# Optimization experiments

Measured on AMD Instinct MI355X. Metric: run time of the kernel, lower is better.

Reference implementation:

```python
import jax, jax.numpy as jnp
import numpy as np

HEADS = 8
DIM_HEAD = 64
SCALE = DIM_HEAD ** -0.5
EPS = 1e-12  # F.normalize default eps


def setup_inputs() -> dict:
    key = jax.random.key(0)
    ks = jax.random.split(key, 4)
    B, C, H, W = 16, 256, 64, 64
    hidden = HEADS * DIM_HEAD  # 512
    x = jax.random.normal(ks[0], (B, C, H, W), dtype=jnp.float32)
    w_qkv = jax.random.normal(ks[1], (3 * hidden, C), dtype=jnp.float32) * (C ** -0.5)
    w_out = jax.random.normal(ks[2], (C, hidden), dtype=jnp.float32) * (hidden ** -0.5)
    b_out = jax.random.normal(ks[3], (C,), dtype=jnp.float32) * 0.01
    g = jnp.ones((1, C, 1, 1), dtype=jnp.float32)
    return {"x": x, "w_qkv": w_qkv, "w_out": w_out, "b_out": b_out, "g": g}


def reference(x, w_qkv, w_out, b_out, g):
    B, C, H, W = x.shape
    N = H * W
    hidden = HEADS * DIM_HEAD
    # 1x1 conv == channel matmul: [B, 3*hidden, N]
    qkv = jnp.einsum('oc,bcn->bon', w_qkv, x.reshape(B, C, N))
    qkv = qkv.reshape(B, 3, HEADS, DIM_HEAD, N)
    q, k, v = qkv[:, 0], qkv[:, 1], qkv[:, 2]  # each [B, h, d, N]
    q = jax.nn.softmax(q, axis=2) * SCALE      # softmax over channel dim d
    k = jax.nn.softmax(k, axis=3)              # softmax over spatial dim n
    context = jnp.einsum('bhdn,bhen->bhde', k, v)   # [B, h, d, e]
    out = jnp.einsum('bhde,bhdn->bhen', context, q) # [B, h, e, N]
    out = out.reshape(B, hidden, N)
    # to_out: 1x1 conv with bias
    y = jnp.einsum('oc,bcn->bon', w_out, out) + b_out[None, :, None]
    y = y.reshape(B, C, H, W)
    # RMSNorm: F.normalize over channel dim, * g * sqrt(W) (x.shape[-1] == width)
    norm = jnp.sqrt(jnp.sum(y * y, axis=1, keepdims=True))
    y = y / jnp.maximum(norm, EPS)
    return y * g * (W ** 0.5)
```

## Files before the change

### kernel.cpp

```cpp
#include <hip/hip_runtime.h>
#include <hip/hip_bf16.h>

#define NPIX 4096
#define CIN  256
#define HID  512
#define QROWS 1536
#define NB   16

typedef unsigned int u32;
typedef unsigned short u16;
typedef float f32x4 __attribute__((ext_vector_type(4)));
typedef short bf16x8 __attribute__((ext_vector_type(8)));

__device__ __forceinline__ float bf2f(u16 u){
  union { u32 i; float f; } v; v.i = ((u32)u) << 16; return v.f;
}
__device__ __forceinline__ u16 f2bf(float f){
  union { float f; u32 u; } v; v.f = f;
  u32 r = v.u + 0x7fffu + ((v.u >> 16) & 1u);
  return (u16)(r >> 16);
}
__device__ __forceinline__ u32 pkbf(float a, float b){
  __hip_bfloat162 h = __float22bfloat162_rn(make_float2(a, b));
  union { __hip_bfloat162 h; u32 u; } cv; cv.h = h; return cv.u;
}
__device__ __forceinline__ void gload16(const u16* g, u16* l){
  __builtin_amdgcn_global_load_lds(
      (const __attribute__((address_space(1))) void*)g,
      (__attribute__((address_space(3))) void*)l, 16, 0, 0);
}

__global__ void k_marker(float* y, int n){
  int i = blockIdx.x * 256 + threadIdx.x;
  if (i < n) y[i] = 1.0e6f;
}

__global__ __launch_bounds__(256) void k_cvt(const float* __restrict__ src,
                                             u16* __restrict__ dst){
  const int i = (blockIdx.x * 256 + threadIdx.x) * 8;
  const float4 a = *(const float4*)(src + i);
  const float4 b = *(const float4*)(src + i + 4);
  *(uint4*)(dst + i) = make_uint4(pkbf(a.x,a.y), pkbf(a.z,a.w),
                                  pkbf(b.x,b.y), pkbf(b.z,b.w));
}

__global__ __launch_bounds__(256) void k_xt(const float* __restrict__ X,
                                            u16* __restrict__ Xt){
  __shared__ float ls[64][67];
  const int n0 = blockIdx.x * 64, c0 = blockIdx.y * 64, b = blockIdx.z;
  const int tid = threadIdx.x;
  const float* Xb = X + (size_t)b * CIN * NPIX;

  {
    const int r = tid >> 2, cq = (tid & 3) * 16;
    #pragma unroll
    for (int j = 0; j < 4; ++j)
      *(float4*)&ls[r][cq + j*4] = *(const float4*)&Xb[(size_t)(c0 + r) * NPIX + n0 + cq + j*4];
  }
  __syncthreads();
  {
    const int nr = tid >> 2, cs = (tid & 3) * 16;
    u32 pk[8];
    #pragma unroll
    for (int j = 0; j < 8; ++j)
      pk[j] = pkbf(ls[cs + 2*j][nr], ls[cs + 2*j + 1][nr]);
    u16* dst = Xt + (size_t)b * NPIX * CIN + (size_t)(n0 + nr) * CIN + c0 + cs;
    *(uint4*)(dst)     = make_uint4(pk[0], pk[1], pk[2], pk[3]);
    *(uint4*)(dst + 8) = make_uint4(pk[4], pk[5], pk[6], pk[7]);
  }
}

__global__ __launch_bounds__(256, 3) void k_qkv(
    const u16* __restrict__ Wq, const u16* __restrict__ Xt, u16* __restrict__ QKV)
{
  __shared__ __align__(16) u16 pool[17408];
  u16* As = pool;
  u16* Bs = pool + 8192;

  const int flat = blockIdx.x;
  const int virt = (flat & 7) * 768 + (flat >> 3);
  const int o0 = (virt % 12) * 128;
  const int n0 = ((virt / 12) & 31) * 128;
  const int b  = virt / 384;

  const int tid = threadIdx.x;
  const int lane = tid & 63;
  const int wv = tid >> 6;
  const int wr = wv >> 1, wc = wv & 1;
  const int g  = lane >> 4;
  const int c  = lane & 15;
  const u16* Xb = Xt + (size_t)b * NPIX * CIN;

  const int grow = lane >> 3;
  const int gch  = (lane & 7) * 8;

  f32x4 acc[4][4];
  #pragma unroll
  for (int i = 0; i < 4; ++i)
    #pragma unroll
    for (int j = 0; j < 4; ++j) acc[i][j] = (f32x4){0.f, 0.f, 0.f, 0.f};

  for (int s = 0; s < 4; ++s) {
    const int k0 = s * 64;
    #pragma unroll
    for (int i = 0; i < 4; ++i) {
      const int j = wv * 4 + i;
      const int row = j * 8 + grow;
      gload16(&Xb[(size_t)(n0 + row) * CIN + k0 + gch], &As[j * 512]);
      gload16(&Wq[(size_t)(o0 + row) * CIN + k0 + gch], &Bs[j * 512]);
    }
    __syncthreads();

    #pragma unroll
    for (int ks = 0; ks < 2; ++ks) {
      bf16x8 af[4], bfr[4];
      #pragma unroll
      for (int mf = 0; mf < 4; ++mf)
        af[mf] = *(const bf16x8*)&As[(wr * 64 + mf * 16 + c) * 64 + ks * 32 + g * 8];
      #pragma unroll
      for (int nf = 0; nf < 4; ++nf)
        bfr[nf] = *(const bf16x8*)&Bs[(wc * 64 + nf * 16 + c) * 64 + ks * 32 + g * 8];
      #pragma unroll
      for (int mf = 0; mf < 4; ++mf)
        #pragma unroll
        for (int nf = 0; nf < 4; ++nf)
          acc[mf][nf] = __builtin_amdgcn_mfma_f32_16x16x32_bf16(
              af[mf], bfr[nf], acc[mf][nf], 0, 0, 0);
    }
    __syncthreads();
  }

  #pragma unroll
  for (int mf = 0; mf < 4; ++mf) {
    const int nrow = wr * 64 + mf * 16 + g * 4;
    #pragma unroll
    for (int nf = 0; nf < 4; ++nf) {
      const int ocol = wc * 64 + nf * 16 + c;
      #pragma unroll
      for (int r = 0; r < 4; ++r)
        pool[ocol * 136 + nrow + r] = f2bf(acc[mf][nf][r]);
    }
  }
  __syncthreads();
  u16* dst = QKV + (size_t)b * QROWS * NPIX;
  #pragma unroll
  for (int i = 0; i < 8; ++i) {
    const int f2 = i * 256 + tid;
    const int orow = f2 >> 4, ch = f2 & 15;
    const uint4 v = *(const uint4*)&pool[orow * 136 + ch * 8];
    *(uint4*)&dst[(size_t)(o0 + orow) * NPIX + n0 + ch * 8] = v;
  }
}

__global__ __launch_bounds__(256) void k_ctx(const u16* __restrict__ QKV,
    float* __restrict__ ctxp, float* __restrict__ Sp)
{
  __shared__ __align__(16) u16 ks[64 * 72];
  __shared__ __align__(16) u16 vs[64 * 72];
  const int split = blockIdx.x, h = blockIdx.y, b = blockIdx.z;
  const int tid = threadIdx.x;
  const int lane = tid & 63, wv = tid >> 6;
  const int g = lane >> 4, c = lane & 15;
  const u16* kb = QKV + ((size_t)b * QROWS + HID     + h * 64) * NPIX;
  const u16* vb = QKV + ((size_t)b * QROWS + 2 * HID + h * 64) * NPIX;

  const int srow = tid >> 2;
  const int sch  = (tid & 3) * 16;

  f32x4 acc[4];
  #pragma unroll
  for (int j = 0; j < 4; ++j) acc[j] = (f32x4){0.f, 0.f, 0.f, 0.f};
  float s_part = 0.f;

  for (int t = 0; t < 16; ++t) {
    const int n0 = split * 1024 + t * 64;
    {
      const uint4 r0 = *(const uint4*)(kb + (size_t)srow * NPIX + n0 + sch);
      const uint4 r1 = *(const uint4*)(kb + (size_t)srow * NPIX + n0 + sch + 8);
      const u32 w[8] = {r0.x, r0.y, r0.z, r0.w, r1.x, r1.y, r1.z, r1.w};
      u32 pk[8];
      #pragma unroll
      for (int j = 0; j < 8; ++j) {
        const float lo = __expf(bf2f((u16)(w[j] & 0xffff)));
        const float hi = __expf(bf2f((u16)(w[j] >> 16)));
        s_part += lo + hi;
        pk[j] = pkbf(lo, hi);
      }
      *(uint4*)&ks[srow * 72 + sch]     = make_uint4(pk[0], pk[1], pk[2], pk[3]);
      *(uint4*)&ks[srow * 72 + sch + 8] = make_uint4(pk[4], pk[5], pk[6], pk[7]);
      const uint4 v0 = *(const uint4*)(vb + (size_t)srow * NPIX + n0 + sch);
      const uint4 v1 = *(const uint4*)(vb + (size_t)srow * NPIX + n0 + sch + 8);
      *(uint4*)&vs[srow * 72 + sch]     = v0;
      *(uint4*)&vs[srow * 72 + sch + 8] = v1;
    }
    __syncthreads();
    #pragma unroll
    for (int ks2 = 0; ks2 < 2; ++ks2) {
      const bf16x8 af = *(const bf16x8*)&ks[(wv * 16 + c) * 72 + ks2 * 32 + g * 8];
      #pragma unroll
      for (int nf = 0; nf < 4; ++nf) {
        const bf16x8 bf = *(const bf16x8*)&vs[(nf * 16 + c) * 72 + ks2 * 32 + g * 8];
        acc[nf] = __builtin_amdgcn_mfma_f32_16x16x32_bf16(af, bf, acc[nf], 0, 0, 0);
      }
    }
    __syncthreads();
  }
  s_part += __shfl_xor(s_part, 1, 64);
  s_part += __shfl_xor(s_part, 2, 64);
  if ((tid & 3) == 0)
    Sp[(size_t)split * 8192 + (b * 8 + h) * 64 + srow] = s_part;

  float* dst = ctxp + (size_t)split * (NB*8*64*64) + ((size_t)(b*8+h)) * 4096;
  #pragma unroll
  for (int nf = 0; nf < 4; ++nf)
    #pragma unroll
    for (int r = 0; r < 4; ++r)
      dst[(wv*16 + g*4 + r) * 64 + nf*16 + c] = acc[nf][r];
}

__global__ __launch_bounds__(256) void k_ctxred(const float* __restrict__ ctxp,
                                                const float* __restrict__ Sp,
                                                float* __restrict__ ctx)
{
  const int SZ = NB*8*64*64;
  const int i = (blockIdx.x * 256 + threadIdx.x) * 4;
  const int bh = i >> 12, d = (i >> 6) & 63;
  const int si = bh * 64 + d;
  const float S = Sp[si] + Sp[8192 + si] + Sp[16384 + si] + Sp[24576 + si];
  const float inv = 1.0f / S;
  float4 a  = *(const float4*)(ctxp + i);
  const float4 c1 = *(const float4*)(ctxp + SZ   + i);
  const float4 c2 = *(const float4*)(ctxp + 2*SZ + i);
  const float4 c3 = *(const float4*)(ctxp + 3*SZ + i);
  a.x = (a.x + c1.x + c2.x + c3.x) * inv;
  a.y = (a.y + c1.y + c2.y + c3.y) * inv;
  a.z = (a.z + c1.z + c2.z + c3.z) * inv;
  a.w = (a.w + c1.w + c2.w + c3.w) * inv;
  *(float4*)(ctx + i) = a;
}

__global__ __launch_bounds__(256) void k_qctx(u16* __restrict__ QKV,
    const float* __restrict__ ctx)
{
  __shared__ __align__(16) u16 As[256 * 72];
  __shared__ __align__(16) u16 Bs[64 * 72];
  const int nt = blockIdx.x, h = blockIdx.y, b = blockIdx.z;
  const int n0 = nt * 256;
  const int tid = threadIdx.x;
  const int lane = tid & 63, wv = tid >> 6;
  const int g = lane >> 4, c = lane & 15;

  const float* cbase = ctx + ((size_t)(b*8+h)) * 4096;
  #pragma unroll
  for (int j = 0; j < 16; ++j) {
    const int idx = tid + j * 256;
    const int d = idx >> 6, e = idx & 63;
    Bs[e * 72 + d] = f2bf(cbase[idx]);
  }

  const u16* qb = QKV + ((size_t)b*QROWS + h*64) * NPIX;
  float vals[64];
  float mx = -3.0e38f;
  #pragma unroll
  for (int d = 0; d < 64; ++d) {
    vals[d] = bf2f(qb[(size_t)d * NPIX + n0 + tid]);
    mx = fmaxf(mx, vals[d]);
  }
  float s = 0.f;
  #pragma unroll
  for (int d = 0; d < 64; ++d) { vals[d] = __expf(vals[d] - mx); s += vals[d]; }
  const float sc = 0.125f / s;
  #pragma unroll
  for (int q = 0; q < 8; ++q) {
    u32 pk[4];
    #pragma unroll
    for (int p = 0; p < 4; ++p)
      pk[p] = pkbf(vals[q*8 + 2*p] * sc, vals[q*8 + 2*p + 1] * sc);
    *(uint4*)&As[tid * 72 + q * 8] = make_uint4(pk[0], pk[1], pk[2], pk[3]);
  }
  __syncthreads();

  f32x4 acc[4][4];
  #pragma unroll
  for (int i = 0; i < 4; ++i)
    #pragma unroll
    for (int j = 0; j < 4; ++j) acc[i][j] = (f32x4){0.f, 0.f, 0.f, 0.f};
  #pragma unroll
  for (int ks = 0; ks < 2; ++ks) {
    bf16x8 af[4], bfr[4];
    #pragma unroll
    for (int mf = 0; mf < 4; ++mf)
      af[mf] = *(const bf16x8*)&As[(wv * 64 + mf * 16 + c) * 72 + ks * 32 + g * 8];
    #pragma unroll
    for (int nf = 0; nf < 4; ++nf)
      bfr[nf] = *(const bf16x8*)&Bs[(nf * 16 + c) * 72 + ks * 32 + g * 8];
    #pragma unroll
    for (int mf = 0; mf < 4; ++mf)
      #pragma unroll
      for (int nf = 0; nf < 4; ++nf)
        acc[mf][nf] = __builtin_amdgcn_mfma_f32_16x16x32_bf16(
            af[mf], bfr[nf], acc[mf][nf], 0, 0, 0);
  }
  __syncthreads();

  u16* pool = As;
  #pragma unroll
  for (int mf = 0; mf < 4; ++mf) {
    const int nrow = wv * 64 + mf * 16 + g * 4;
    #pragma unroll
    for (int nf = 0; nf < 4; ++nf) {
      const int ecol = nf * 16 + c;
      #pragma unroll
      for (int r = 0; r < 4; ++r)
        pool[ecol * 264 + nrow + r] = f2bf(acc[mf][nf][r]);
    }
  }
  __syncthreads();
  u16* ob = QKV + ((size_t)b*QROWS + h*64) * NPIX;
  #pragma unroll
  for (int i = 0; i < 8; ++i) {
    const int f2 = i * 256 + tid;
    const int erow = f2 >> 5, ch = f2 & 31;
    const uint4 v = *(const uint4*)&pool[erow * 264 + ch * 8];
    *(uint4*)&ob[(size_t)erow * NPIX + n0 + ch * 8] = v;
  }
}

__global__ __launch_bounds__(256) void k_proj(const u16* __restrict__ QKV,
    const u16* __restrict__ Wbf, const float* __restrict__ bo,
    const float* __restrict__ gg, float* __restrict__ Y)
{
  __shared__ __align__(16) u16 As[256][72];
  __shared__ __align__(16) u16 Bs[64][72];
  __shared__ float red[4][64];
  __shared__ float sbias[256], sgain[256];
  const int nt = blockIdx.x, b = blockIdx.y;
  const int n0 = nt * 64;
  const int tid = threadIdx.x;
  const int lane = tid & 63, wv = tid >> 6;
  const int g = lane >> 4, c = lane & 15;
  const u16* ob = QKV + (size_t)b * QROWS * NPIX;

  sbias[tid] = bo[tid];
  sgain[tid] = gg[tid];

  f32x4 acc[4][4];
  #pragma unroll
  for (int i = 0; i < 4; ++i)
    #pragma unroll
    for (int j = 0; j < 4; ++j) acc[i][j] = (f32x4){0.f, 0.f, 0.f, 0.f};

  for (int s = 0; s < 8; ++s) {
    const int k0 = s * 64;
    #pragma unroll
    for (int i = 0; i < 8; ++i) {
      const int flat = i * 256 + tid;
      const int row = flat >> 3, kc = flat & 7;
      *(uint4*)&As[row][kc * 8] =
          *(const uint4*)&Wbf[(size_t)row * HID + k0 + kc * 8];
    }
    {
      const int kb0 = wv * 16;
      u16 vals[16];
      #pragma unroll
      for (int kk = 0; kk < 16; ++kk)
        vals[kk] = ob[(size_t)(k0 + kb0 + kk) * NPIX + n0 + lane];
      u32 pk[8];
      #pragma unroll
      for (int j = 0; j < 8; ++j)
        pk[j] = (u32)vals[2*j] | ((u32)vals[2*j+1] << 16);
      *(uint4*)&Bs[lane][kb0]     = make_uint4(pk[0], pk[1], pk[2], pk[3]);
      *(uint4*)&Bs[lane][kb0 + 8] = make_uint4(pk[4], pk[5], pk[6], pk[7]);
    }
    __syncthreads();

    #pragma unroll
    for (int ks = 0; ks < 2; ++ks) {
      bf16x8 af[4], bfr[4];
      #pragma unroll
      for (int mf = 0; mf < 4; ++mf)
        af[mf] = *(const bf16x8*)&As[wv * 64 + mf * 16 + c][ks * 32 + g * 8];
      #pragma unroll
      for (int nf = 0; nf < 4; ++nf)
        bfr[nf] = *(const bf16x8*)&Bs[nf * 16 + c][ks * 32 + g * 8];
      #pragma unroll
      for (int mf = 0; mf < 4; ++mf)
        #pragma unroll
        for (int nf = 0; nf < 4; ++nf)
          acc[mf][nf] = __builtin_amdgcn_mfma_f32_16x16x32_bf16(
              af[mf], bfr[nf], acc[mf][nf], 0, 0, 0);
    }
    __syncthreads();
  }

  #pragma unroll
  for (int mf = 0; mf < 4; ++mf)
    #pragma unroll
    for (int r = 0; r < 4; ++r) {
      const float bb = sbias[wv * 64 + mf * 16 + g * 4 + r];
      #pragma unroll
      for (int nf = 0; nf < 4; ++nf) acc[mf][nf][r] += bb;
    }

  #pragma unroll
  for (int nf = 0; nf < 4; ++nf) {
    float v = 0.f;
    #pragma unroll
    for (int mf = 0; mf < 4; ++mf)
      #pragma unroll
      for (int r = 0; r < 4; ++r)
        v = fmaf(acc[mf][nf][r], acc[mf][nf][r], v);
    v += __shfl_xor(v, 16, 64);
    v += __shfl_xor(v, 32, 64);
    if (g == 0) red[wv][nf * 16 + c] = v;
  }
  __syncthreads();
  float scale[4];
  #pragma unroll
  for (int nf = 0; nf < 4; ++nf) {
    const int col = nf * 16 + c;
    const float tot = red[0][col] + red[1][col] + red[2][col] + red[3][col];
    scale[nf] = 8.0f / fmaxf(sqrtf(tot), 1e-12f);
  }

  float* yb = Y + (size_t)b * CIN * NPIX;
  #pragma unroll
  for (int mf = 0; mf < 4; ++mf)
    #pragma unroll
    for (int r = 0; r < 4; ++r) {
      const int row = wv * 64 + mf * 16 + g * 4 + r;
      const float gr = sgain[row];
      #pragma unroll
      for (int nf = 0; nf < 4; ++nf)
        yb[(size_t)row * NPIX + n0 + nf * 16 + c] = acc[mf][nf][r] * scale[nf] * gr;
    }
}

extern "C" void kernel_launch(void* const* d_in, const int* in_sizes, int n_in,
                              void* d_out, int out_size, void* d_ws, size_t ws_size,
                              hipStream_t stream) {
  const float* x     = (const float*)d_in[0];
  const float* w_qkv = (const float*)d_in[1];
  const float* w_out = (const float*)d_in[2];
  const float* b_out = (const float*)d_in[3];
  const float* g     = (const float*)d_in[4];
  float* y = (float*)d_out;

  char* ws = (char*)d_ws;
  u16*    qkv   = (u16*)(ws);
  u16*    xt    = (u16*)(ws + 201326592);
  float*  ctx   = (float*)(ws + 201392128);
  float*  ctxp  = (float*)(ws + 203489280);
  float*  Sp    = (float*)(ws + 211877888);
  u16*    wbf   = (u16*)(ws + 234881024);
  u16*    wqb   = (u16*)(ws + 235143168);

  if (ws_size < 235929600) {
    k_marker<<<dim3((out_size + 255) / 256), 256, 0, stream>>>(y, out_size);
    return;
  }

  k_cvt   <<<dim3(64),         256, 0, stream>>>(w_out, wbf);
  k_cvt   <<<dim3(192),        256, 0, stream>>>(w_qkv, wqb);
  k_xt    <<<dim3(64, 4, 16),  256, 0, stream>>>(x, xt);
  k_qkv   <<<dim3(6144),       256, 0, stream>>>(wqb, xt, qkv);
  k_ctx   <<<dim3(4, 8, 16),   256, 0, stream>>>(qkv, ctxp, Sp);
  k_ctxred<<<dim3(512),        256, 0, stream>>>(ctxp, Sp, ctx);
  k_qctx  <<<dim3(16, 8, 16),  256, 0, stream>>>(qkv, ctx);
  k_proj  <<<dim3(64, 16),     256, 0, stream>>>(qkv, wbf, b_out, g, y);
}
```

Baseline: 192.8 us.

## Double-buffer LDS tiles in QKV GEMM to overlap global loads with MFMA

The QKV projection kernel now prefetches the next K-slice of X and W into a second LDS buffer while computing on the current one, using explicit vmcnt waits and raw barriers instead of __syncthreads. This is meant to hide global-to-LDS load latency behind MFMA work. LDS use doubles to 64KB per block, so launch bounds drop from 3 to 2 blocks per CU, which reduces occupancy.

Result: slower. 198.9 us (median of 2 runs) (+3.2%).

```diff
diff --git a/kernel.cpp b/kernel.cpp
--- a/kernel.cpp
+++ b/kernel.cpp
@@ -70,12 +70,10 @@
   }
 }
 
-__global__ __launch_bounds__(256, 3) void k_qkv(
+__global__ __launch_bounds__(256, 2) void k_qkv(
     const u16* __restrict__ Wq, const u16* __restrict__ Xt, u16* __restrict__ QKV)
 {
-  __shared__ __align__(16) u16 pool[17408];
-  u16* As = pool;
-  u16* Bs = pool + 8192;
+  __shared__ __align__(16) u16 lds[32768];
 
   const int flat = blockIdx.x;
   const int virt = (flat & 7) * 768 + (flat >> 3);
@@ -100,17 +98,41 @@
     #pragma unroll
     for (int j = 0; j < 4; ++j) acc[i][j] = (f32x4){0.f, 0.f, 0.f, 0.f};
 
-  for (int s = 0; s < 4; ++s) {
-    const int k0 = s * 64;
+  {
+    u16* As = lds;
+    u16* Bs = lds + 8192;
     #pragma unroll
     for (int i = 0; i < 4; ++i) {
       const int j = wv * 4 + i;
       const int row = j * 8 + grow;
-      gload16(&Xb[(size_t)(n0 + row) * CIN + k0 + gch], &As[j * 512]);
-      gload16(&Wq[(size_t)(o0 + row) * CIN + k0 + gch], &Bs[j * 512]);
-    }
-    __syncthreads();
-
+      gload16(&Xb[(size_t)(n0 + row) * CIN + gch], &As[j * 512]);
+      gload16(&Wq[(size_t)(o0 + row) * CIN + gch], &Bs[j * 512]);
+    }
+  }
+
+  #pragma unroll
+  for (int s = 0; s < 4; ++s) {
+    const int cur = s & 1;
+    if (s < 3) {
+      const int k0 = (s + 1) * 64;
+      u16* As = lds + (cur ^ 1) * 16384;
+      u16* Bs = As + 8192;
+      #pragma unroll
+      for (int i = 0; i < 4; ++i) {
+        const int j = wv * 4 + i;
+        const int row = j * 8 + grow;
+        gload16(&Xb[(size_t)(n0 + row) * CIN + k0 + gch], &As[j * 512]);
+        gload16(&Wq[(size_t)(o0 + row) * CIN + k0 + gch], &Bs[j * 512]);
+      }
+      asm volatile("s_waitcnt vmcnt(8)" ::: "memory");
+    } else {
+      asm volatile("s_waitcnt vmcnt(0)" ::: "memory");
+    }
+    __builtin_amdgcn_s_barrier();
+    __builtin_amdgcn_sched_barrier(0);
+
+    const u16* As = lds + cur * 16384;
+    const u16* Bs = As + 8192;
     #pragma unroll
     for (int ks = 0; ks < 2; ++ks) {
       bf16x8 af[4], bfr[4];
@@ -127,9 +149,10 @@
           acc[mf][nf] = __builtin_amdgcn_mfma_f32_16x16x32_bf16(
               af[mf], bfr[nf], acc[mf][nf], 0, 0, 0);
     }
-    __syncthreads();
-  }
-
+    __builtin_amdgcn_s_barrier();
+  }
+
+  u16* pool = lds;
   #pragma unroll
   for (int mf = 0; mf < 4; ++mf) {
     const int nrow = wr * 64 + mf * 16 + g * 4;
```
